# Performance work log

Measured on AMD Instinct MI355X. Metric: run time of the kernel, lower is better.

The kernel has to match this reference:

```python
import jax, jax.numpy as jnp
import numpy as np


def setup_inputs() -> dict:
    key = jax.random.key(0)
    k1, k2 = jax.random.split(key)
    N, C, H, W = 8, 256, 96, 96
    Cw, KK = 32, 9  # groups=8 -> C_w = C/8; ks=3 -> K*K=9
    x = jax.random.normal(k1, (N, C, H, W), dtype=jnp.float32)
    w = jax.random.normal(k2, (N, Cw, KK, H, W), dtype=jnp.float32)
    return {"x": x, "w": w}


def reference(x, w):
    # x: (N, C, H, W); w: (N, C_w, K*K, H, W)
    N, C, H, W = x.shape
    Cw, KK = w.shape[1], w.shape[2]
    K = int(np.sqrt(KK))
    pad = (K - 1) // 2
    G = C // Cw
    xp = jnp.pad(x, ((0, 0), (0, 0), (pad, pad), (pad, pad)))
    out = jnp.zeros((N, G, Cw, H, W), dtype=x.dtype)
    # accumulate over the K*K taps without materializing the full window tensor;
    # window index k = a*K + b corresponds to xp[..., h+a, w+b]
    for k in range(KK):
        a, b = divmod(k, K)
        win = xp[:, :, a:a + H, b:b + W].reshape(N, G, Cw, H, W)
        out = out + win * w[:, None, :, k]
    return out.reshape(N, C, H, W)
```

## Files before the change

### kernel.cpp

```cpp
#include <hip/hip_runtime.h>


#define N_  8
#define C_  256
#define H_  96
#define W_  96
#define CW_ 32
#define G_  8

typedef float f32x4 __attribute__((ext_vector_type(4)));

__global__ __launch_bounds__(256, 4) void SKA_kernel(const float* __restrict__ x,
                                                     const float* __restrict__ wgt,
                                                     float* __restrict__ out) {
    constexpr size_t PLANE = (size_t)H_ * W_;

    const int tid   = threadIdx.x;
    const int widx  = tid & 31;
    const int rowid = tid >> 5;
    const int lane  = tid & 63;

    const int blk = blockIdx.x;
    const int ht  = blk % (H_ / 8);
    const int t1  = blk / (H_ / 8);
    const int cw  = t1 % CW_;
    const int n   = t1 / CW_;
    const int h   = ht * 8 + rowid;
    const int w0  = widx * 4;

    if (widx >= 24) return;

    const float* wb = wgt + (((size_t)(n * CW_ + cw) * 9) * H_ + (size_t)h) * W_ + w0;
    f32x4 wv[9];
#pragma unroll
    for (int k = 0; k < 9; ++k)
        wv[k] = *reinterpret_cast<const f32x4*>(wb + (size_t)k * PLANE);

    float acc[G_][4];
#pragma unroll
    for (int g = 0; g < G_; ++g)
#pragma unroll
        for (int j = 0; j < 4; ++j) acc[g][j] = 0.f;

    const float* xb = x + ((size_t)n * C_ + cw) * PLANE + w0;

#pragma unroll
    for (int a = 0; a < 3; ++a) {
        const int hh = h + a - 1;
        if (hh < 0 || hh >= H_) continue;
        const f32x4 w0v = wv[a * 3 + 0];
        const f32x4 w1v = wv[a * 3 + 1];
        const f32x4 w2v = wv[a * 3 + 2];
#pragma unroll
        for (int g = 0; g < G_; ++g) {
            const f32x4 xm = *reinterpret_cast<const f32x4*>(
                xb + (size_t)(g * CW_) * PLANE + (size_t)hh * W_);
            float xl = __shfl(xm.w, lane - 1);
            float xr = __shfl(xm.x, lane + 1);
            xl = (widx == 0) ? 0.f : xl;
            xr = (widx == 23) ? 0.f : xr;
            acc[g][0] = fmaf(xl,   w0v.x, acc[g][0]);
            acc[g][0] = fmaf(xm.x, w1v.x, acc[g][0]);
            acc[g][0] = fmaf(xm.y, w2v.x, acc[g][0]);
            acc[g][1] = fmaf(xm.x, w0v.y, acc[g][1]);
            acc[g][1] = fmaf(xm.y, w1v.y, acc[g][1]);
            acc[g][1] = fmaf(xm.z, w2v.y, acc[g][1]);
            acc[g][2] = fmaf(xm.y, w0v.z, acc[g][2]);
            acc[g][2] = fmaf(xm.z, w1v.z, acc[g][2]);
            acc[g][2] = fmaf(xm.w, w2v.z, acc[g][2]);
            acc[g][3] = fmaf(xm.z, w0v.w, acc[g][3]);
            acc[g][3] = fmaf(xm.w, w1v.w, acc[g][3]);
            acc[g][3] = fmaf(xr,   w2v.w, acc[g][3]);
        }
    }

    float* ob = out + ((size_t)n * C_ + cw) * PLANE + (size_t)h * W_ + w0;
#pragma unroll
    for (int g = 0; g < G_; ++g) {
        f32x4 v;
        v.x = acc[g][0]; v.y = acc[g][1]; v.z = acc[g][2]; v.w = acc[g][3];
        __builtin_nontemporal_store(v, reinterpret_cast<f32x4*>(ob + (size_t)(g * CW_) * PLANE));
    }
}

extern "C" void kernel_launch(void* const* d_in, const int* in_sizes, int n_in,
                              void* d_out, int out_size, void* d_ws, size_t ws_size,
                              hipStream_t stream) {
    const float* x   = (const float*)d_in[0];
    const float* wgt = (const float*)d_in[1];
    float* out = (float*)d_out;

    constexpr int grid = N_ * CW_ * (H_ / 8);
    SKA_kernel<<<grid, 256, 0, stream>>>(x, wgt, out);
}
```

Baseline: 42.83 us.

## Stage input rows into LDS via direct global-to-LDS loads with 64-thread blocks

```diff
diff --git a/kernel.cpp b/kernel.cpp
--- a/kernel.cpp
+++ b/kernel.cpp
@@ -1,4 +1,5 @@
 #include <hip/hip_runtime.h>
+#include <stdint.h>
 
 
 #define N_  8
@@ -7,79 +8,104 @@
 #define W_  96
 #define CW_ 32
 #define G_  8
+#define PL_ (H_ * W_)
 
 typedef float f32x4 __attribute__((ext_vector_type(4)));
 
-__global__ __launch_bounds__(256, 4) void SKA_kernel(const float* __restrict__ x,
-                                                     const float* __restrict__ wgt,
-                                                     float* __restrict__ out) {
-    constexpr size_t PLANE = (size_t)H_ * W_;
+__global__ __launch_bounds__(64, 4) void SKA_kernel(const float* __restrict__ x,
+                                                    const float* __restrict__ wgt,
+                                                    float* __restrict__ out) {
+    __shared__ float xs[4 * G_ * W_];
 
-    const int tid   = threadIdx.x;
-    const int widx  = tid & 31;
-    const int rowid = tid >> 5;
-    const int lane  = tid & 63;
+    const int lane  = threadIdx.x;
+    const int widx  = lane & 31;
+    const int rowid = lane >> 5;
 
-    const int blk = blockIdx.x;
-    const int ht  = blk % (H_ / 8);
-    const int t1  = blk / (H_ / 8);
-    const int cw  = t1 % CW_;
-    const int n   = t1 / CW_;
-    const int h   = ht * 8 + rowid;
-    const int w0  = widx * 4;
+    const int b  = blockIdx.x;
+    const int lb = (b & 7) * 1536 + (b >> 3);
+    const int ht = lb % 48;
+    const int t1 = lb / 48;
+    const int cw = t1 % CW_;
+    const int n  = t1 / CW_;
+    const int h0 = ht * 2;
+    const int h  = h0 + rowid;
+    const int w0a = widx * 4;
+    const int w0  = (w0a > W_ - 4) ? (W_ - 4) : w0a;
+    const bool active = (widx < 24);
 
-    if (widx >= 24) return;
-
-    const float* wb = wgt + (((size_t)(n * CW_ + cw) * 9) * H_ + (size_t)h) * W_ + w0;
+    const float* wb = wgt + (size_t)(((n * CW_ + cw) * 9) * H_ + h) * W_ + w0;
     f32x4 wv[9];
 #pragma unroll
     for (int k = 0; k < 9; ++k)
-        wv[k] = *reinterpret_cast<const f32x4*>(wb + (size_t)k * PLANE);
+        wv[k] = __builtin_nontemporal_load(reinterpret_cast<const f32x4*>(wb + k * PL_));
 
-    float acc[G_][4];
+    const int nc = (n * C_ + cw) * PL_;
+    int goff[3], csel[3];
 #pragma unroll
-    for (int g = 0; g < G_; ++g)
+    for (int cc = 0; cc < 3; ++cc) {
+        const int wo = cc * 256 + lane * 4;
+        goff[cc] = (wo / 96) * (CW_ * PL_);
+        csel[cc] = wo % 96;
+    }
 #pragma unroll
-        for (int j = 0; j < 4; ++j) acc[g][j] = 0.f;
+    for (int r = 0; r < 4; ++r) {
+        int row = h0 - 1 + r;
+        row = row < 0 ? 0 : (row > H_ - 1 ? H_ - 1 : row);
+#pragma unroll
+        for (int cc = 0; cc < 3; ++cc) {
+            const int off = nc + goff[cc] + row * W_ + csel[cc];
+            const uint32_t lds_off = (uint32_t)(uintptr_t)&xs[(r * 3 + cc) * 256];
+            __builtin_amdgcn_global_load_lds(
+                (const __attribute__((address_space(1))) void*)(uintptr_t)(x + off),
+                (__attribute__((address_space(3))) void*)lds_off,
+                16, 0, 0);
+        }
+    }
 
-    const float* xb = x + ((size_t)n * C_ + cw) * PLANE + w0;
+    __builtin_amdgcn_sched_barrier(0);
+    asm volatile("s_waitcnt vmcnt(0)" ::: "memory");
+    __builtin_amdgcn_sched_barrier(0);
+
+    f32x4 acc[G_];
+#pragma unroll
+    for (int g = 0; g < G_; ++g) acc[g] = (f32x4)(0.f);
 
 #pragma unroll
     for (int a = 0; a < 3; ++a) {
         const int hh = h + a - 1;
         if (hh < 0 || hh >= H_) continue;
-        const f32x4 w0v = wv[a * 3 + 0];
-        const f32x4 w1v = wv[a * 3 + 1];
-        const f32x4 w2v = wv[a * 3 + 2];
+        const f32x4 wa = wv[a * 3 + 0];
+        const f32x4 wm = wv[a * 3 + 1];
+        const f32x4 wc = wv[a * 3 + 2];
 #pragma unroll
         for (int g = 0; g < G_; ++g) {
             const f32x4 xm = *reinterpret_cast<const f32x4*>(
-                xb + (size_t)(g * CW_) * PLANE + (size_t)hh * W_);
+                &xs[(rowid + a) * (G_ * W_) + g * W_ + w0]);
             float xl = __shfl(xm.w, lane - 1);
             float xr = __shfl(xm.x, lane + 1);
             xl = (widx == 0) ? 0.f : xl;
             xr = (widx == 23) ? 0.f : xr;
-            acc[g][0] = fmaf(xl,   w0v.x, acc[g][0]);
-            acc[g][0] = fmaf(xm.x, w1v.x, acc[g][0]);
-            acc[g][0] = fmaf(xm.y, w2v.x, acc[g][0]);
-            acc[g][1] = fmaf(xm.x, w0v.y, acc[g][1]);
-            acc[g][1] = fmaf(xm.y, w1v.y, acc[g][1]);
-            acc[g][1] = fmaf(xm.z, w2v.y, acc[g][1]);
-            acc[g][2] = fmaf(xm.y, w0v.z, acc[g][2]);
-            acc[g][2] = fmaf(xm.z, w1v.z, acc[g][2]);
-            acc[g][2] = fmaf(xm.w, w2v.z, acc[g][2]);
-            acc[g][3] = fmaf(xm.z, w0v.w, acc[g][3]);
-            acc[g][3] = fmaf(xm.w, w1v.w, acc[g][3]);
-            acc[g][3] = fmaf(xr,   w2v.w, acc[g][3]);
+            acc[g].x = fmaf(xl,   wa.x, acc[g].x);
+            acc[g].x = fmaf(xm.x, wm.x, acc[g].x);
+            acc[g].x = fmaf(xm.y, wc.x, acc[g].x);
+            acc[g].y = fmaf(xm.x, wa.y, acc[g].y);
+            acc[g].y = fmaf(xm.y, wm.y, acc[g].y);
+            acc[g].y = fmaf(xm.z, wc.y, acc[g].y);
+            acc[g].z = fmaf(xm.y, wa.z, acc[g].z);
+            acc[g].z = fmaf(xm.z, wm.z, acc[g].z);
+            acc[g].z = fmaf(xm.w, wc.z, acc[g].z);
+            acc[g].w = fmaf(xm.z, wa.w, acc[g].w);
+            acc[g].w = fmaf(xm.w, wm.w, acc[g].w);
+            acc[g].w = fmaf(xr,   wc.w, acc[g].w);
         }
     }
 
-    float* ob = out + ((size_t)n * C_ + cw) * PLANE + (size_t)h * W_ + w0;
+    if (active) {
+        float* ob = out + nc + h * W_ + w0a;
 #pragma unroll
-    for (int g = 0; g < G_; ++g) {
-        f32x4 v;
-        v.x = acc[g][0]; v.y = acc[g][1]; v.z = acc[g][2]; v.w = acc[g][3];
-        __builtin_nontemporal_store(v, reinterpret_cast<f32x4*>(ob + (size_t)(g * CW_) * PLANE));
+        for (int g = 0; g < G_; ++g)
+            __builtin_nontemporal_store(acc[g],
+                reinterpret_cast<f32x4*>(ob + g * (CW_ * PL_)));
     }
 }
 
@@ -90,6 +116,6 @@
     const float* wgt = (const float*)d_in[1];
     float* out = (float*)d_out;
 
-    constexpr int grid = N_ * CW_ * (H_ / 8);
-    SKA_kernel<<<grid, 256, 0, stream>>>(x, wgt, out);
+    constexpr int grid = N_ * CW_ * (H_ / 2);
+    SKA_kernel<<<grid, 64, 0, stream>>>(x, wgt, out);
 }
```

New measurement: 43.91 us. 2.5% more time.
